# Optimization experiments

Hardware: AMD Instinct MI355X
Metric: run time of the kernel (lower is better)

Reference implementation:

```python
import jax, jax.numpy as jnp
import numpy as np

N = 50000
E_DIR = 200000
KEEP = 320000  # int(0.8 * 2 * E_DIR) after to_undirected + dropout_edge(p=0.2)
IN, OUT, HID = 128, 256, 512
G = 512  # number of graphs
BN_EPS = 1e-5


def setup_inputs() -> dict:
    rng = np.random.default_rng(0)
    x = jnp.asarray(rng.standard_normal((N, IN)).astype(np.float32))
    src = rng.integers(0, N, E_DIR)
    dst = rng.integers(0, N, E_DIR)
    ei = np.stack([src, dst]).astype(np.int64)
    und = np.concatenate([ei, ei[::-1]], axis=1)  # to_undirected -> [2, 2E]
    edge_index1 = jnp.asarray(und[:, rng.permutation(2 * E_DIR)[:KEEP]])
    edge_index2 = jnp.asarray(und[:, rng.permutation(2 * E_DIR)[:KEEP]])
    mask1 = jnp.asarray(rng.permutation(N) < N // 2)
    mask2 = jnp.asarray(rng.permutation(N) < N // 2)
    batch = jnp.asarray(np.sort(rng.integers(0, G, N)).astype(np.int32))

    def w(i, o):
        return jnp.asarray((rng.standard_normal((i, o)) / np.sqrt(i)).astype(np.float32))

    ones = lambda d: jnp.ones((d,), jnp.float32)
    zeros = lambda d: jnp.zeros((d,), jnp.float32)
    return dict(
        x=x, edge_index1=edge_index1, edge_index2=edge_index2,
        mask1=mask1, mask2=mask2, batch=batch,
        e0_w1=w(IN, HID), e0_w2=w(HID, OUT), e0_bg=ones(HID), e0_bb=zeros(HID), e0_ng=ones(OUT), e0_nb=zeros(OUT),
        e1_w1=w(OUT, HID), e1_w2=w(HID, OUT), e1_bg=ones(HID), e1_bb=zeros(HID), e1_ng=ones(OUT), e1_nb=zeros(OUT),
        d_w1=w(OUT, HID), d_w2=w(HID, IN), d_bg=ones(HID), d_bb=zeros(HID), d_ng=ones(IN), d_nb=zeros(IN),
    )


def _bn(h, g, b):  # BatchNorm1d, training mode (batch stats, biased var)
    mu = h.mean(0)
    var = h.var(0)
    return g * (h - mu) * jax.lax.rsqrt(var + BN_EPS) + b


def _gin(xn, ei, w1, w2, bg, bb):
    # GINConv(eps=0): mlp(x + sum_{j in N(i)} x_j); messages flow src->dst
    agg = jax.ops.segment_sum(xn[ei[0]], ei[1], num_segments=xn.shape[0])
    h = xn + agg
    return jax.nn.relu(_bn(h @ w1, bg, bb)) @ w2


def _encoder(xn, ei, batch, layers):
    pooled = []
    for (w1, w2, bg, bb, ng, nb) in layers:
        xn = jax.nn.relu(_bn(_gin(xn, ei, w1, w2, bg, bb), ng, nb))
        pooled.append(jax.ops.segment_sum(xn, batch, num_segments=G))  # global_add_pool
    return xn, jnp.concatenate(pooled, axis=1)


def _cos(a, b):  # F.normalize(p=2) dot product, eps=1e-12
    an = a / jnp.maximum(jnp.linalg.norm(a, axis=-1, keepdims=True), 1e-12)
    bn_ = b / jnp.maximum(jnp.linalg.norm(b, axis=-1, keepdims=True), 1e-12)
    return (an * bn_).sum(-1)


def reference(x, edge_index1, edge_index2, mask1, mask2, batch,
              e0_w1, e0_w2, e0_bg, e0_bb, e0_ng, e0_nb,
              e1_w1, e1_w2, e1_bg, e1_bb, e1_ng, e1_nb,
              d_w1, d_w2, d_bg, d_bb, d_ng, d_nb):
    enc = [(e0_w1, e0_w2, e0_bg, e0_bb, e0_ng, e0_nb),
           (e1_w1, e1_w2, e1_bg, e1_bb, e1_ng, e1_nb)]
    dec = [(d_w1, d_w2, d_bg, d_bb, d_ng, d_nb)]

    def _pass(ei, mb):
        m = mb[:, None]
        x1 = jnp.where(m, 0.0, x)
        h, _gh = _encoder(x1, ei, batch, enc)
        re_h = jnp.where(m, 0.0, h)
        re_x, _ = _encoder(re_h, ei, batch, dec)
        w = mb.astype(x.dtype)
        # sce_loss(alpha=1) restricted to masked rows, target detached
        l = jnp.sum(w * (1.0 - _cos(re_x, jax.lax.stop_gradient(x)))) / jnp.sum(w)
        return re_x, l

    re_x1, loss1 = _pass(edge_index1, mask1)
    re_x2, loss2 = _pass(edge_index2, mask2)
    cl_loss = jnp.mean(1.0 - _cos(re_x2, re_x1))
    return loss1 + loss2 + 0.1 * cl_loss
```

## Files before the change

### kernel.cpp

```cpp
#include <hip/hip_runtime.h>
#include <hip/hip_bf16.h>
#include <cstdint>

#define NN 50000
#define NEDGE 320000

#define K_F32 0
#define K_BF16 1
#define K_IN 2

typedef __attribute__((ext_vector_type(8))) short bf16x8;
typedef __attribute__((ext_vector_type(4))) float f32x4;

__device__ __forceinline__ float bf2f(unsigned short u) {
  return __uint_as_float(((unsigned)u) << 16);
}
__device__ __forceinline__ unsigned short f2bf(float f) {
  unsigned u = __float_as_uint(f);
  unsigned r = ((u >> 16) & 1u) + 0x7FFFu;
  return (unsigned short)((u + r) >> 16);
}
__device__ __forceinline__ float load1f(const void* p, size_t i, int isbf) {
  return isbf ? bf2f(((const unsigned short*)p)[i]) : ((const float*)p)[i];
}
__device__ __forceinline__ int maskAt(const void* m, int i, int u8) {
  return u8 ? (int)((const unsigned char*)m)[i] : ((const int*)m)[i];
}

__global__ void sniff_kernel(const void* bg, const void* mask, const void* ei, int* flags) {
  if (threadIdx.x == 0 && blockIdx.x == 0) {
    unsigned w = *(const unsigned*)bg;
    flags[0] = (w == 0x3F800000u) ? 0 : 1;
    const unsigned char* mb = (const unsigned char*)mask;
    int u8 = 0;
    for (int i = 0; i < 1024; ++i)
      if ((i & 3) && mb[i]) { u8 = 1; break; }
    flags[1] = u8;
    const int* ew = (const int*)ei;
    int i64 = 1;
    for (int i = 0; i < 256; ++i)
      if (ew[2 * i + 1] != 0) { i64 = 0; break; }
    flags[2] = i64;
  }
}

__global__ void diag_kernel(void* out, float v) {
  if (threadIdx.x == 0 && blockIdx.x == 0) ((unsigned short*)out)[0] = f2bf(v);
}

__global__ void transpose_w(const void* __restrict__ W, const int* __restrict__ flags,
                            unsigned short* __restrict__ Wt, int K, int Ko) {
  int idx = blockIdx.x * 256 + threadIdx.x;
  if (idx >= K * Ko) return;
  int n = idx / K, k = idx - n * K;
  Wt[idx] = f2bf(load1f(W, (size_t)k * Ko + n, flags[0]));
}

__global__ void csr_hist(const void* __restrict__ eip, const int* __restrict__ flags,
                         int* __restrict__ deg) {
  int e = blockIdx.x * 256 + threadIdx.x;
  if (e >= NEDGE) return;
  int d = flags[2] ? (int)((const long long*)eip)[NEDGE + e] : ((const int*)eip)[NEDGE + e];
  atomicAdd(deg + d, 1);
}

__global__ void scan1(const int* __restrict__ deg, int* __restrict__ rowptr,
                      int* __restrict__ bsum) {
  __shared__ int sm[256];
  int t = threadIdx.x, i = blockIdx.x * 256 + t;
  int v = (i < NN) ? deg[i] : 0;
  sm[t] = v; __syncthreads();
  for (int o = 1; o < 256; o <<= 1) {
    int y = (t >= o) ? sm[t - o] : 0;
    __syncthreads();
    sm[t] += y;
    __syncthreads();
  }
  if (i < NN) rowptr[i] = sm[t] - v;
  if (t == 255) bsum[blockIdx.x] = sm[255];
}

__global__ void scan2(int* __restrict__ bsum, int nb) {
  __shared__ int sm[256];
  int t = threadIdx.x;
  int v = (t < nb) ? bsum[t] : 0;
  sm[t] = v; __syncthreads();
  for (int o = 1; o < 256; o <<= 1) {
    int y = (t >= o) ? sm[t - o] : 0;
    __syncthreads();
    sm[t] += y;
    __syncthreads();
  }
  bsum[t] = sm[t] - v;
}

__global__ void scan3(int* __restrict__ rowptr, const int* __restrict__ bsum,
                      int* __restrict__ cursor) {
  int i = blockIdx.x * 256 + threadIdx.x;
  if (i < NN) {
    int r = rowptr[i] + bsum[blockIdx.x];
    rowptr[i] = r;
    cursor[i] = r;
  } else if (i == NN) {
    rowptr[NN] = NEDGE;
  }
}

__global__ void csr_fill(const void* __restrict__ eip, const int* __restrict__ flags,
                         int* __restrict__ cursor, int* __restrict__ adj) {
  int e = blockIdx.x * 256 + threadIdx.x;
  if (e >= NEDGE) return;
  int s, d;
  if (flags[2]) {
    s = (int)((const long long*)eip)[e];
    d = (int)((const long long*)eip)[NEDGE + e];
  } else {
    s = ((const int*)eip)[e];
    d = ((const int*)eip)[NEDGE + e];
  }
  int pos = atomicAdd(cursor + d, 1);
  adj[pos] = s;
}

template<int F, bool MASKED, bool BN, bool ISBF>
__device__ __forceinline__ void gf_body(const void* __restrict__ feat,
                                        const void* __restrict__ maskp,
                                        const int* __restrict__ adj,
                                        int s0, int s1, int v, int lane, int mu8,
                                        const float* __restrict__ sc,
                                        const float* __restrict__ sh,
                                        float* __restrict__ a) {
  constexpr int VEC = F / 64;
  auto ld = [&](int r, float* t) {
    size_t gb = (size_t)r * F + lane * VEC;
    if (ISBF) {
      if (VEC == 4) {
        ushort4 h = *(const ushort4*)((const unsigned short*)feat + gb);
        t[0] = bf2f(h.x); t[1] = bf2f(h.y); t[2] = bf2f(h.z); t[3] = bf2f(h.w);
      } else {
        ushort2 h = *(const ushort2*)((const unsigned short*)feat + gb);
        t[0] = bf2f(h.x); t[1] = bf2f(h.y);
      }
    } else {
      if (VEC == 4) {
        float4 h = *(const float4*)((const float*)feat + gb);
        t[0] = h.x; t[1] = h.y; t[2] = h.z; t[3] = h.w;
      } else {
        float2 h = *(const float2*)((const float*)feat + gb);
        t[0] = h.x; t[1] = h.y;
      }
    }
    if (BN) {
#pragma unroll
      for (int i = 0; i < VEC; ++i) t[i] = fmaxf(0.f, t[i] * sc[i] + sh[i]);
    }
  };
  {
    float t[VEC];
    ld(v, t);
    float m = (MASKED && maskAt(maskp, v, mu8)) ? 0.f : 1.f;
#pragma unroll
    for (int i = 0; i < VEC; ++i) a[i] = m * t[i];
  }
  int e = s0;
  for (; e + 4 <= s1; e += 4) {
    int n0 = adj[e], n1 = adj[e + 1], n2 = adj[e + 2], n3 = adj[e + 3];
    float m0 = 1.f, m1 = 1.f, m2 = 1.f, m3 = 1.f;
    if (MASKED) {
      m0 = maskAt(maskp, n0, mu8) ? 0.f : 1.f;
      m1 = maskAt(maskp, n1, mu8) ? 0.f : 1.f;
      m2 = maskAt(maskp, n2, mu8) ? 0.f : 1.f;
      m3 = maskAt(maskp, n3, mu8) ? 0.f : 1.f;
    }
    float t0[VEC], t1[VEC], t2[VEC], t3[VEC];
    ld(n0, t0); ld(n1, t1); ld(n2, t2); ld(n3, t3);
#pragma unroll
    for (int i = 0; i < VEC; ++i)
      a[i] += m0 * t0[i] + m1 * t1[i] + m2 * t2[i] + m3 * t3[i];
  }
  for (; e < s1; ++e) {
    int s = adj[e];
    if (MASKED && maskAt(maskp, s, mu8)) continue;
    float t[VEC];
    ld(s, t);
#pragma unroll
    for (int i = 0; i < VEC; ++i) a[i] += t[i];
  }
}

template<int F, bool MASKED, bool BN>
__launch_bounds__(256)
__global__ void gather_fused(const void* __restrict__ feat, int kind,
                             const void* __restrict__ maskp,
                             const int* __restrict__ rowptr, const int* __restrict__ adj,
                             const float* __restrict__ ss,
                             const int* __restrict__ flags,
                             unsigned short* __restrict__ outH) {
  constexpr int VEC = F / 64;
  int v = (blockIdx.x * 256 + threadIdx.x) >> 6;
  if (v >= NN) return;
  int lane = threadIdx.x & 63;
  int mu8 = flags[1];
  float sc[VEC], sh[VEC];
  if (BN) {
#pragma unroll
    for (int i = 0; i < VEC; ++i) {
      sc[i] = ss[lane * VEC + i];
      sh[i] = ss[F + lane * VEC + i];
    }
  }
  float a[VEC];
  int s0 = rowptr[v], s1 = rowptr[v + 1];
  int fbf = (kind == K_IN) ? flags[0] : kind;
  if (fbf) gf_body<F, MASKED, BN, true>(feat, maskp, adj, s0, s1, v, lane, mu8, sc, sh, a);
  else     gf_body<F, MASKED, BN, false>(feat, maskp, adj, s0, s1, v, lane, mu8, sc, sh, a);
  size_t ob = (size_t)v * F + lane * VEC;
  if (VEC == 4) {
    ushort4 o; o.x = f2bf(a[0]); o.y = f2bf(a[1]); o.z = f2bf(a[2]); o.w = f2bf(a[3]);
    *(ushort4*)(outH + ob) = o;
  } else {
    ushort2 o; o.x = f2bf(a[0]); o.y = f2bf(a[1]);
    *(ushort2*)(outH + ob) = o;
  }
}

template<int K, int KO, int SPLIT, bool BNF>
__launch_bounds__(256)
__global__ void gemm_mfma(const unsigned short* __restrict__ A,
                          const float* __restrict__ ss,
                          const unsigned short* __restrict__ Wt,
                          unsigned short* __restrict__ Cout,
                          float* __restrict__ stats) {
  constexpr int NTW = KO / (SPLIT * 64);
  constexpr int NC = K / 32;
  constexpr int BD = (NTW <= 2) ? 3 : 2;
  __shared__ __align__(16) unsigned short As[2][64 * 40];
  const int tid = threadIdx.x;
  const int row0 = blockIdx.x * 64;
  const int colBase = blockIdx.y * (KO / SPLIT);
  const int srow = tid >> 2;
  const int sk = (tid & 3) * 8;
  const int grow = row0 + srow;
  const bool valid = grow < NN;
  const int wv = tid >> 6, lane = tid & 63;
  const int l15 = lane & 15, quad = lane >> 4;
  const int n0 = colBase + wv * (KO / SPLIT / 4);
  f32x4 zero = {0.f, 0.f, 0.f, 0.f};
  f32x4 acc[4][NTW];
#pragma unroll
  for (int m = 0; m < 4; ++m)
#pragma unroll
    for (int nt = 0; nt < NTW; ++nt) acc[m][nt] = zero;

  ushort4 pbh[2][2];
  bf16x8 breg[BD][NTW];

  auto issue_A = [&](int kt, int set) {
    if (!valid) return;
    const ushort4* P = (const ushort4*)(A + (size_t)grow * K + kt + sk);
    pbh[set][0] = P[0]; pbh[set][1] = P[1];
  };
  auto issue_B = [&](int kt, int buf) {
#pragma unroll
    for (int nt = 0; nt < NTW; ++nt)
      breg[buf][nt] = *(const bf16x8*)(Wt + (size_t)(n0 + nt * 16 + l15) * K + kt + quad * 8);
  };
  auto transform_store = [&](int kt, int set, unsigned short* buf) {
    float v[8];
    if (valid) {
#pragma unroll
      for (int i = 0; i < 2; ++i) {
        v[4 * i] = bf2f(pbh[set][i].x); v[4 * i + 1] = bf2f(pbh[set][i].y);
        v[4 * i + 2] = bf2f(pbh[set][i].z); v[4 * i + 3] = bf2f(pbh[set][i].w);
      }
      if (BNF) {
        int j = kt + sk;
#pragma unroll
        for (int i = 0; i < 8; ++i)
          v[i] = fmaxf(0.f, v[i] * ss[j + i] + ss[K + j + i]);
      }
    } else {
#pragma unroll
      for (int i = 0; i < 8; ++i) v[i] = 0.f;
    }
    unsigned short* dst = buf + srow * 40 + sk;
#pragma unroll
    for (int i = 0; i < 2; ++i) {
      ushort4 o;
      o.x = f2bf(v[4 * i]); o.y = f2bf(v[4 * i + 1]);
      o.z = f2bf(v[4 * i + 2]); o.w = f2bf(v[4 * i + 3]);
      *(ushort4*)(dst + 4 * i) = o;
    }
  };

  issue_A(0, 0);
  transform_store(0, 0, As[0]);
  if (NC > 1) issue_A(32, 1);
  if (NC > 2) issue_A(64, 0);
  issue_B(0, 0);
  if (NC > 1) issue_B(32, 1);
  __syncthreads();

#pragma unroll
  for (int i = 0; i < NC; ++i) {
    const int kt = i << 5;
    if (i + 1 < NC) transform_store(kt + 32, (i + 1) & 1, As[(i + 1) & 1]);
    if (i + 3 < NC) issue_A(kt + 96, (i + 3) & 1);
    if (i + 2 < NC) issue_B(kt + 64, (i + 2) % BD);
    bf16x8 afr[4];
#pragma unroll
    for (int m = 0; m < 4; ++m)
      afr[m] = *(const bf16x8*)(As[i & 1] + (m * 16 + l15) * 40 + quad * 8);
#pragma unroll
    for (int nt = 0; nt < NTW; ++nt)
#pragma unroll
      for (int m = 0; m < 4; ++m)
        acc[m][nt] = __builtin_amdgcn_mfma_f32_16x16x32_bf16(afr[m], breg[i % BD][nt], acc[m][nt], 0, 0, 0);
    __syncthreads();
  }

#pragma unroll
  for (int m = 0; m < 4; ++m)
#pragma unroll
    for (int r = 0; r < 4; ++r) {
      int gr = row0 + m * 16 + quad * 4 + r;
      if (gr < NN) {
        size_t ob = (size_t)gr * KO + n0 + l15;
#pragma unroll
        for (int nt = 0; nt < NTW; ++nt)
          Cout[ob + nt * 16] = f2bf(acc[m][nt][r]);
      }
    }

#pragma unroll
  for (int nt = 0; nt < NTW; ++nt) {
    float s = 0.f, q = 0.f;
#pragma unroll
    for (int m = 0; m < 4; ++m)
#pragma unroll
      for (int r = 0; r < 4; ++r) {
        float vv = acc[m][nt][r];
        s += vv; q += vv * vv;
      }
    s += __shfl_xor(s, 16); s += __shfl_xor(s, 32);
    q += __shfl_xor(q, 16); q += __shfl_xor(q, 32);
    if (quad == 0) {
      int col = n0 + nt * 16 + l15;
      atomicAdd(stats + col, s);
      atomicAdd(stats + KO + col, q);
    }
  }
}

__global__ void bn_finalize(const float* __restrict__ sums, const void* __restrict__ g,
                            const void* __restrict__ b, const int* __restrict__ flags,
                            float* __restrict__ ss, int Ko) {
  int c = blockIdx.x * blockDim.x + threadIdx.x;
  if (c < Ko) {
    const float invN = 1.f / (float)NN;
    float mu = sums[c] * invN;
    float var = sums[Ko + c] * invN - mu * mu;
    float sc = load1f(g, c, flags[0]) * rsqrtf(var + 1e-5f);
    ss[c] = sc;
    ss[Ko + c] = load1f(b, c, flags[0]) - mu * sc;
  }
}

template<bool CL>
__launch_bounds__(256)
__global__ void loss_kernel(const unsigned short* __restrict__ u2, const float* __restrict__ ss,
                            const void* __restrict__ xp, const void* __restrict__ maskp,
                            const unsigned short* __restrict__ r1,
                            const int* __restrict__ flags,
                            unsigned short* __restrict__ rx, float* __restrict__ accb,
                            float* __restrict__ accb_cl) {
  __shared__ float redS[4], redC[4], redL[4];
  const int lane = threadIdx.x & 63;
  const int wv = threadIdx.x >> 6;
  const int g = lane >> 4, li = lane & 15;
  const int r = blockIdx.x * 16 + wv * 4 + g;
  const int fbf = flags[0], mu8 = flags[1];
  const int j0 = li * 8;
  size_t ofs = (size_t)r * 128 + j0;

  float a[8], xv[8], cv[8];
  {
    uint4 h = *(const uint4*)(u2 + ofs);
    unsigned hw[4] = {h.x, h.y, h.z, h.w};
#pragma unroll
    for (int i = 0; i < 4; ++i) {
      a[2 * i]     = bf2f((unsigned short)(hw[i] & 0xFFFF));
      a[2 * i + 1] = bf2f((unsigned short)(hw[i] >> 16));
    }
  }
#pragma unroll
  for (int i = 0; i < 8; ++i)
    a[i] = fmaxf(0.f, a[i] * ss[j0 + i] + ss[128 + j0 + i]);
  {
    uint4 o;
    unsigned ow[4];
#pragma unroll
    for (int i = 0; i < 4; ++i) {
      unsigned short lo = f2bf(a[2 * i]), hi = f2bf(a[2 * i + 1]);
      a[2 * i] = bf2f(lo); a[2 * i + 1] = bf2f(hi);
      ow[i] = (unsigned)lo | ((unsigned)hi << 16);
    }
    o.x = ow[0]; o.y = ow[1]; o.z = ow[2]; o.w = ow[3];
    *(uint4*)(rx + ofs) = o;
  }
  if (fbf) {
    uint4 h = *(const uint4*)((const unsigned short*)xp + ofs);
    unsigned hw[4] = {h.x, h.y, h.z, h.w};
#pragma unroll
    for (int i = 0; i < 4; ++i) {
      xv[2 * i]     = bf2f((unsigned short)(hw[i] & 0xFFFF));
      xv[2 * i + 1] = bf2f((unsigned short)(hw[i] >> 16));
    }
  } else {
    const float* xf = (const float*)xp + ofs;
    float4 h0 = *(const float4*)xf;
    float4 h1 = *(const float4*)(xf + 4);
    xv[0] = h0.x; xv[1] = h0.y; xv[2] = h0.z; xv[3] = h0.w;
    xv[4] = h1.x; xv[5] = h1.y; xv[6] = h1.z; xv[7] = h1.w;
  }
  if (CL) {
    uint4 h = *(const uint4*)(r1 + ofs);
    unsigned hw[4] = {h.x, h.y, h.z, h.w};
#pragma unroll
    for (int i = 0; i < 4; ++i) {
      cv[2 * i]     = bf2f((unsigned short)(hw[i] & 0xFFFF));
      cv[2 * i + 1] = bf2f((unsigned short)(hw[i] >> 16));
    }
  }
  float dot = 0.f, na = 0.f, nx = 0.f, dotc = 0.f, nc = 0.f;
#pragma unroll
  for (int i = 0; i < 8; ++i) {
    dot += a[i] * xv[i];
    na  += a[i] * a[i];
    nx  += xv[i] * xv[i];
    if (CL) { dotc += a[i] * cv[i]; nc += cv[i] * cv[i]; }
  }
#pragma unroll
  for (int off = 1; off < 16; off <<= 1) {
    dot += __shfl_xor(dot, off);
    na  += __shfl_xor(na, off);
    nx  += __shfl_xor(nx, off);
    if (CL) { dotc += __shfl_xor(dotc, off); nc += __shfl_xor(nc, off); }
  }
  float cs = dot / (fmaxf(sqrtf(na), 1e-12f) * fmaxf(sqrtf(nx), 1e-12f));
  float lsum = 0.f, lcnt = 0.f, clsum = 0.f;
  if (maskAt(maskp, r, mu8)) { lsum = 1.f - cs; lcnt = 1.f; }
  if (CL) {
    float csc = dotc / (fmaxf(sqrtf(na), 1e-12f) * fmaxf(sqrtf(nc), 1e-12f));
    clsum = 1.f - csc;
  }
  lsum += __shfl_xor(lsum, 16); lsum += __shfl_xor(lsum, 32);
  lcnt += __shfl_xor(lcnt, 16); lcnt += __shfl_xor(lcnt, 32);
  if (CL) { clsum += __shfl_xor(clsum, 16); clsum += __shfl_xor(clsum, 32); }
  if (lane == 0) { redS[wv] = lsum; redC[wv] = lcnt; if (CL) redL[wv] = clsum; }
  __syncthreads();
  if (threadIdx.x == 0) {
    int bin = (blockIdx.x & 63) * 16;
    atomicAdd(&accb[bin], redS[0] + redS[1] + redS[2] + redS[3]);
    atomicAdd(&accb[1024 + bin], redC[0] + redC[1] + redC[2] + redC[3]);
    if (CL) atomicAdd(&accb_cl[bin], redL[0] + redL[1] + redL[2] + redL[3]);
  }
}

__global__ void final_kernel(const float* __restrict__ acc, void* __restrict__ out,
                             const int* __restrict__ flags) {
  int lane = threadIdx.x & 63;
  float v0 = acc[lane * 16], v1 = acc[1024 + lane * 16], v2 = acc[2048 + lane * 16];
  float v3 = acc[3072 + lane * 16], v4 = acc[4096 + lane * 16];
#pragma unroll
  for (int off = 32; off > 0; off >>= 1) {
    v0 += __shfl_xor(v0, off);
    v1 += __shfl_xor(v1, off);
    v2 += __shfl_xor(v2, off);
    v3 += __shfl_xor(v3, off);
    v4 += __shfl_xor(v4, off);
  }
  if (threadIdx.x == 0 && blockIdx.x == 0) {
    float v = v0 / v1 + v2 / v3 + 0.1f * (v4 / (float)NN);
    if (flags[0]) ((unsigned short*)out)[0] = f2bf(v);
    else          ((float*)out)[0] = v;
  }
}

extern "C" void kernel_launch(void* const* d_in, const int* in_sizes, int n_in,
                              void* d_out, int out_size, void* d_ws, size_t ws_size,
                              hipStream_t stream) {
  const void* x   = d_in[0];
  const void* ei1 = d_in[1];
  const void* ei2 = d_in[2];
  const void* m1  = d_in[3];
  const void* m2  = d_in[4];
  const void* e0_w1 = d_in[6],  *e0_w2 = d_in[7],  *e0_bg = d_in[8],  *e0_bb = d_in[9];
  const void* e0_ng = d_in[10], *e0_nb = d_in[11];
  const void* e1_w1 = d_in[12], *e1_w2 = d_in[13], *e1_bg = d_in[14], *e1_bb = d_in[15];
  const void* e1_ng = d_in[16], *e1_nb = d_in[17];
  const void* dw1 = d_in[18], *dw2 = d_in[19], *dbg = d_in[20], *dbb = d_in[21];
  const void* dng = d_in[22], *dnb = d_in[23];

  char* p = (char*)d_ws;
  const size_t OFS_T      = 0;
  const size_t OFS_H      = OFS_T      + (size_t)NN * 512 * 2;
  const size_t OFS_U      = OFS_H      + (size_t)NN * 256 * 2;
  const size_t OFS_RX1    = OFS_U      + (size_t)NN * 256 * 2;
  const size_t OFS_RX2    = OFS_RX1    + (size_t)NN * 128 * 2;
  const size_t OFS_WT     = OFS_RX2    + (size_t)NN * 128 * 2;
  const size_t OFS_ROWPTR = OFS_WT     + 655360 * 2;
  const size_t OFS_CURSOR = OFS_ROWPTR + 50016 * 4;
  const size_t OFS_ADJ    = OFS_CURSOR + 50016 * 4;
  const size_t OFS_BSUM   = OFS_ADJ    + (size_t)NEDGE * 4;
  const size_t OFS_STATS  = OFS_BSUM   + 256 * 4;
  const size_t OFS_SS     = OFS_STATS  + 6 * 1024 * 4;
  const size_t OFS_ACC    = OFS_SS     + 1024 * 4;
  const size_t OFS_FLAGS  = OFS_ACC    + 5120 * 4;
  const size_t NEED       = OFS_FLAGS + 16;

  if (ws_size < NEED) {
    diag_kernel<<<1, 64, 0, stream>>>(d_out, (float)(ws_size >> 20));
    return;
  }

  unsigned short* T   = (unsigned short*)(p + OFS_T);
  unsigned short* H   = (unsigned short*)(p + OFS_H);
  unsigned short* U   = (unsigned short*)(p + OFS_U);
  unsigned short* RX1 = (unsigned short*)(p + OFS_RX1);
  unsigned short* RX2 = (unsigned short*)(p + OFS_RX2);
  unsigned short* WT  = (unsigned short*)(p + OFS_WT);
  int* rowptr = (int*)(p + OFS_ROWPTR);
  int* cursor = (int*)(p + OFS_CURSOR);
  int* adj    = (int*)(p + OFS_ADJ);
  int* bsum   = (int*)(p + OFS_BSUM);
  float* stats = (float*)(p + OFS_STATS);
  float* ss    = (float*)(p + OFS_SS);
  float* acc   = (float*)(p + OFS_ACC);
  int*   flags = (int*)(p + OFS_FLAGS);

  const int EB = (NEDGE + 255) / 256;
  const int SB = (NN + 255) / 256;
  const int GB = (NN + 63) / 64;
  const int WB = (NN + 3) / 4;
  const int LB = NN / 16;
  const dim3 gS2(GB, 2), gS1(GB, 1);

  hipMemsetAsync(acc, 0, 5120 * sizeof(float) + 4 * sizeof(int), stream);
  sniff_kernel<<<1, 64, 0, stream>>>(e0_bg, m1, ei1, flags);

  transpose_w<<<(128 * 512 + 255) / 256, 256, 0, stream>>>(e0_w1, flags, WT + 0,      128, 512);
  transpose_w<<<(512 * 256 + 255) / 256, 256, 0, stream>>>(e0_w2, flags, WT + 65536,  512, 256);
  transpose_w<<<(256 * 512 + 255) / 256, 256, 0, stream>>>(e1_w1, flags, WT + 196608, 256, 512);
  transpose_w<<<(512 * 256 + 255) / 256, 256, 0, stream>>>(e1_w2, flags, WT + 327680, 512, 256);
  transpose_w<<<(256 * 512 + 255) / 256, 256, 0, stream>>>(dw1,   flags, WT + 458752, 256, 512);
  transpose_w<<<(512 * 128 + 255) / 256, 256, 0, stream>>>(dw2,   flags, WT + 589824, 512, 128);

  for (int pass = 0; pass < 2; ++pass) {
    const void* ei = pass ? ei2 : ei1;
    const void* mk = pass ? m2 : m1;
    unsigned short* rx = pass ? RX2 : RX1;
    float* accp = acc + 2048 * pass;

    hipMemsetAsync(cursor, 0, 50016 * 4, stream);
    csr_hist<<<EB, 256, 0, stream>>>(ei, flags, cursor);
    scan1<<<SB, 256, 0, stream>>>(cursor, rowptr, bsum);
    scan2<<<1, 256, 0, stream>>>(bsum, SB);
    scan3<<<SB, 256, 0, stream>>>(rowptr, bsum, cursor);
    csr_fill<<<EB, 256, 0, stream>>>(ei, flags, cursor, adj);

    hipMemsetAsync(stats, 0, 6 * 1024 * 4, stream);

    gather_fused<128, true, false><<<WB, 256, 0, stream>>>(x, K_IN, mk, rowptr, adj, nullptr, flags, H);
    gemm_mfma<128, 512, 2, false><<<gS2, 256, 0, stream>>>(H, nullptr, WT + 0, T, stats);
    bn_finalize<<<2, 256, 0, stream>>>(stats, e0_bg, e0_bb, flags, ss, 512);
    gemm_mfma<512, 256, 1, true><<<gS1, 256, 0, stream>>>(T, ss, WT + 65536, U, stats + 1024);
    bn_finalize<<<1, 256, 0, stream>>>(stats + 1024, e0_ng, e0_nb, flags, ss, 256);

    gather_fused<256, false, true><<<WB, 256, 0, stream>>>(U, K_BF16, nullptr, rowptr, adj, ss, flags, H);
    gemm_mfma<256, 512, 2, false><<<gS2, 256, 0, stream>>>(H, nullptr, WT + 196608, T, stats + 2048);
    bn_finalize<<<2, 256, 0, stream>>>(stats + 2048, e1_bg, e1_bb, flags, ss, 512);
    gemm_mfma<512, 256, 1, true><<<gS1, 256, 0, stream>>>(T, ss, WT + 327680, U, stats + 3072);
    bn_finalize<<<1, 256, 0, stream>>>(stats + 3072, e1_ng, e1_nb, flags, ss, 256);

    gather_fused<256, true, true><<<WB, 256, 0, stream>>>(U, K_BF16, mk, rowptr, adj, ss, flags, H);
    gemm_mfma<256, 512, 2, false><<<gS2, 256, 0, stream>>>(H, nullptr, WT + 458752, T, stats + 4096);
    bn_finalize<<<2, 256, 0, stream>>>(stats + 4096, dbg, dbb, flags, ss, 512);
    gemm_mfma<512, 128, 1, true><<<gS1, 256, 0, stream>>>(T, ss, WT + 589824, U, stats + 5120);
    bn_finalize<<<1, 256, 0, stream>>>(stats + 5120, dng, dnb, flags, ss, 128);

    if (pass == 0)
      loss_kernel<false><<<LB, 256, 0, stream>>>(U, ss, x, mk, nullptr, flags, rx, accp, nullptr);
    else
      loss_kernel<true><<<LB, 256, 0, stream>>>(U, ss, x, mk, RX1, flags, rx, accp, acc + 4096);
  }

  final_kernel<<<1, 64, 0, stream>>>(acc, d_out, flags);
}
```

Measured before the change: 1.171 ms.

## Batch both augmentation passes into single kernel launches over stacked rows

Runs the two independent encoder/decoder passes together. Each CSR build, gather, GEMM and BN-finalize launch now covers both passes, with per-pass offsets into doubled row buffers padded to a multiple of 64 rows. The two separate loss kernels become one that computes both reconstruction losses and the contrastive term in a single read, so the re-x buffers are no longer written and read back. This halves the number of launches and doubles grid sizes for better GPU fill, at the cost of twice the workspace memory.

```diff
diff --git a/kernel.cpp b/kernel.cpp
--- a/kernel.cpp
+++ b/kernel.cpp
@@ -3,7 +3,11 @@
 #include <cstdint>
 
 #define NN 50000
+#define NNP 50048
 #define NEDGE 320000
+#define PB (NNP / 64)
+#define EBV 1250
+#define SBV 196
 
 #define K_F32 0
 #define K_BF16 1
@@ -25,6 +29,14 @@
 }
 __device__ __forceinline__ int maskAt(const void* m, int i, int u8) {
   return u8 ? (int)((const unsigned char*)m)[i] : ((const int*)m)[i];
+}
+__device__ __forceinline__ void unpack8(uint4 h, float* t) {
+  unsigned hw[4] = {h.x, h.y, h.z, h.w};
+#pragma unroll
+  for (int i = 0; i < 4; ++i) {
+    t[2 * i]     = bf2f((unsigned short)(hw[i] & 0xFFFF));
+    t[2 * i + 1] = bf2f((unsigned short)(hw[i] >> 16));
+  }
 }
 
 __global__ void sniff_kernel(const void* bg, const void* mask, const void* ei, int* flags) {
@@ -56,19 +68,24 @@
   Wt[idx] = f2bf(load1f(W, (size_t)k * Ko + n, flags[0]));
 }
 
-__global__ void csr_hist(const void* __restrict__ eip, const int* __restrict__ flags,
-                         int* __restrict__ deg) {
-  int e = blockIdx.x * 256 + threadIdx.x;
-  if (e >= NEDGE) return;
+__global__ void csr_hist(const void* __restrict__ e1, const void* __restrict__ e2,
+                         const int* __restrict__ flags, int* __restrict__ deg2) {
+  int eg = blockIdx.x * 256 + threadIdx.x;
+  int p = eg >= NEDGE ? 1 : 0;
+  int e = eg - p * NEDGE;
+  const void* eip = p ? e2 : e1;
   int d = flags[2] ? (int)((const long long*)eip)[NEDGE + e] : ((const int*)eip)[NEDGE + e];
-  atomicAdd(deg + d, 1);
-}
-
-__global__ void scan1(const int* __restrict__ deg, int* __restrict__ rowptr,
-                      int* __restrict__ bsum) {
+  atomicAdd(deg2 + p * 50016 + d, 1);
+}
+
+__global__ void scan1(const int* __restrict__ deg2, int* __restrict__ rowptr2,
+                      int* __restrict__ bsum2) {
   __shared__ int sm[256];
-  int t = threadIdx.x, i = blockIdx.x * 256 + t;
-  int v = (i < NN) ? deg[i] : 0;
+  int t = threadIdx.x;
+  int p = blockIdx.x >= SBV ? 1 : 0;
+  int b = blockIdx.x - p * SBV;
+  int i = b * 256 + t;
+  int v = (i < NN) ? deg2[p * 50016 + i] : 0;
   sm[t] = v; __syncthreads();
   for (int o = 1; o < 256; o <<= 1) {
     int y = (t >= o) ? sm[t - o] : 0;
@@ -76,14 +93,15 @@
     sm[t] += y;
     __syncthreads();
   }
-  if (i < NN) rowptr[i] = sm[t] - v;
-  if (t == 255) bsum[blockIdx.x] = sm[255];
-}
-
-__global__ void scan2(int* __restrict__ bsum, int nb) {
+  if (i < NN) rowptr2[p * 50016 + i] = sm[t] - v;
+  if (t == 255) bsum2[p * 256 + b] = sm[255];
+}
+
+__global__ void scan2(int* __restrict__ bsum2) {
   __shared__ int sm[256];
   int t = threadIdx.x;
-  int v = (t < nb) ? bsum[t] : 0;
+  int* arr = bsum2 + blockIdx.x * 256;
+  int v = (t < SBV) ? arr[t] : 0;
   sm[t] = v; __syncthreads();
   for (int o = 1; o < 256; o <<= 1) {
     int y = (t >= o) ? sm[t - o] : 0;
@@ -91,25 +109,30 @@
     sm[t] += y;
     __syncthreads();
   }
-  bsum[t] = sm[t] - v;
-}
-
-__global__ void scan3(int* __restrict__ rowptr, const int* __restrict__ bsum,
-                      int* __restrict__ cursor) {
-  int i = blockIdx.x * 256 + threadIdx.x;
+  arr[t] = sm[t] - v;
+}
+
+__global__ void scan3(int* __restrict__ rowptr2, const int* __restrict__ bsum2,
+                      int* __restrict__ cursor2) {
+  int p = blockIdx.x >= SBV ? 1 : 0;
+  int b = blockIdx.x - p * SBV;
+  int i = b * 256 + threadIdx.x;
   if (i < NN) {
-    int r = rowptr[i] + bsum[blockIdx.x];
-    rowptr[i] = r;
-    cursor[i] = r;
+    int r = rowptr2[p * 50016 + i] + bsum2[p * 256 + b];
+    rowptr2[p * 50016 + i] = r;
+    cursor2[p * 50016 + i] = r;
   } else if (i == NN) {
-    rowptr[NN] = NEDGE;
-  }
-}
-
-__global__ void csr_fill(const void* __restrict__ eip, const int* __restrict__ flags,
-                         int* __restrict__ cursor, int* __restrict__ adj) {
-  int e = blockIdx.x * 256 + threadIdx.x;
-  if (e >= NEDGE) return;
+    rowptr2[p * 50016 + NN] = NEDGE;
+  }
+}
+
+__global__ void csr_fill(const void* __restrict__ e1, const void* __restrict__ e2,
+                         const int* __restrict__ flags,
+                         int* __restrict__ cursor2, int* __restrict__ adj2) {
+  int eg = blockIdx.x * 256 + threadIdx.x;
+  int p = eg >= NEDGE ? 1 : 0;
+  int e = eg - p * NEDGE;
+  const void* eip = p ? e2 : e1;
   int s, d;
   if (flags[2]) {
     s = (int)((const long long*)eip)[e];
@@ -118,21 +141,23 @@
     s = ((const int*)eip)[e];
     d = ((const int*)eip)[NEDGE + e];
   }
-  int pos = atomicAdd(cursor + d, 1);
-  adj[pos] = s;
-}
-
-template<int F, bool MASKED, bool BN, bool ISBF>
+  int pos = atomicAdd(cursor2 + p * 50016 + d, 1);
+  adj2[p * NEDGE + pos] = s;
+}
+
+template<int F, bool MASKED, bool BN, bool ISBF, bool SHARED>
 __device__ __forceinline__ void gf_body(const void* __restrict__ feat,
                                         const void* __restrict__ maskp,
                                         const int* __restrict__ adj,
-                                        int s0, int s1, int v, int lane, int mu8,
+                                        int s0, int s1, int v, size_t pbase,
+                                        int lane, int mu8,
                                         const float* __restrict__ sc,
                                         const float* __restrict__ sh,
                                         float* __restrict__ a) {
   constexpr int VEC = F / 64;
   auto ld = [&](int r, float* t) {
-    size_t gb = (size_t)r * F + lane * VEC;
+    size_t frow = SHARED ? (size_t)r : (pbase + r);
+    size_t gb = frow * F + lane * VEC;
     if (ISBF) {
       if (VEC == 4) {
         ushort4 h = *(const ushort4*)((const unsigned short*)feat + gb);
@@ -188,33 +213,39 @@
   }
 }
 
-template<int F, bool MASKED, bool BN>
+template<int F, bool MASKED, bool BN, bool SHARED>
 __launch_bounds__(256)
 __global__ void gather_fused(const void* __restrict__ feat, int kind,
-                             const void* __restrict__ maskp,
-                             const int* __restrict__ rowptr, const int* __restrict__ adj,
+                             const void* __restrict__ mk1, const void* __restrict__ mk2,
+                             const int* __restrict__ rowptr2, const int* __restrict__ adj2,
                              const float* __restrict__ ss,
                              const int* __restrict__ flags,
                              unsigned short* __restrict__ outH) {
   constexpr int VEC = F / 64;
-  int v = (blockIdx.x * 256 + threadIdx.x) >> 6;
-  if (v >= NN) return;
+  int w = (blockIdx.x * 256 + threadIdx.x) >> 6;
+  int p = w >= NN ? 1 : 0;
+  int v = w - p * NN;
   int lane = threadIdx.x & 63;
   int mu8 = flags[1];
+  const void* mk = p ? mk2 : mk1;
+  const int* rp_ = rowptr2 + p * 50016;
+  const int* aj = adj2 + p * NEDGE;
+  const float* ssp = ss + p * 2 * F;
+  size_t pbase = (size_t)p * NNP;
   float sc[VEC], sh[VEC];
   if (BN) {
 #pragma unroll
     for (int i = 0; i < VEC; ++i) {
-      sc[i] = ss[lane * VEC + i];
-      sh[i] = ss[F + lane * VEC + i];
+      sc[i] = ssp[lane * VEC + i];
+      sh[i] = ssp[F + lane * VEC + i];
     }
   }
   float a[VEC];
-  int s0 = rowptr[v], s1 = rowptr[v + 1];
+  int s0 = rp_[v], s1 = rp_[v + 1];
   int fbf = (kind == K_IN) ? flags[0] : kind;
-  if (fbf) gf_body<F, MASKED, BN, true>(feat, maskp, adj, s0, s1, v, lane, mu8, sc, sh, a);
-  else     gf_body<F, MASKED, BN, false>(feat, maskp, adj, s0, s1, v, lane, mu8, sc, sh, a);
-  size_t ob = (size_t)v * F + lane * VEC;
+  if (fbf) gf_body<F, MASKED, BN, true, SHARED>(feat, mk, aj, s0, s1, v, pbase, lane, mu8, sc, sh, a);
+  else     gf_body<F, MASKED, BN, false, SHARED>(feat, mk, aj, s0, s1, v, pbase, lane, mu8, sc, sh, a);
+  size_t ob = (pbase + v) * F + lane * VEC;
   if (VEC == 4) {
     ushort4 o; o.x = f2bf(a[0]); o.y = f2bf(a[1]); o.z = f2bf(a[2]); o.w = f2bf(a[3]);
     *(ushort4*)(outH + ob) = o;
@@ -236,15 +267,18 @@
   constexpr int BD = (NTW <= 2) ? 3 : 2;
   __shared__ __align__(16) unsigned short As[2][64 * 40];
   const int tid = threadIdx.x;
+  const int pass = (blockIdx.x >= PB) ? 1 : 0;
   const int row0 = blockIdx.x * 64;
   const int colBase = blockIdx.y * (KO / SPLIT);
   const int srow = tid >> 2;
   const int sk = (tid & 3) * 8;
   const int grow = row0 + srow;
-  const bool valid = grow < NN;
+  const bool valid = (grow - pass * NNP) < NN;
   const int wv = tid >> 6, lane = tid & 63;
   const int l15 = lane & 15, quad = lane >> 4;
   const int n0 = colBase + wv * (KO / SPLIT / 4);
+  const float* ssp = BNF ? (ss + pass * 2 * K) : ss;
+  float* statsp = stats + pass * 1024;
   f32x4 zero = {0.f, 0.f, 0.f, 0.f};
   f32x4 acc[4][NTW];
 #pragma unroll
@@ -277,7 +311,7 @@
         int j = kt + sk;
 #pragma unroll
         for (int i = 0; i < 8; ++i)
-          v[i] = fmaxf(0.f, v[i] * ss[j + i] + ss[K + j + i]);
+          v[i] = fmaxf(0.f, v[i] * ssp[j + i] + ssp[K + j + i]);
       }
     } else {
 #pragma unroll
@@ -324,7 +358,7 @@
 #pragma unroll
     for (int r = 0; r < 4; ++r) {
       int gr = row0 + m * 16 + quad * 4 + r;
-      if (gr < NN) {
+      if (gr - pass * NNP < NN) {
         size_t ob = (size_t)gr * KO + n0 + l15;
 #pragma unroll
         for (int nt = 0; nt < NTW; ++nt)
@@ -346,8 +380,8 @@
     q += __shfl_xor(q, 16); q += __shfl_xor(q, 32);
     if (quad == 0) {
       int col = n0 + nt * 16 + l15;
-      atomicAdd(stats + col, s);
-      atomicAdd(stats + KO + col, q);
+      atomicAdd(statsp + col, s);
+      atomicAdd(statsp + KO + col, q);
     }
   }
 }
@@ -356,114 +390,91 @@
                             const void* __restrict__ b, const int* __restrict__ flags,
                             float* __restrict__ ss, int Ko) {
   int c = blockIdx.x * blockDim.x + threadIdx.x;
+  int p = blockIdx.y;
   if (c < Ko) {
     const float invN = 1.f / (float)NN;
-    float mu = sums[c] * invN;
-    float var = sums[Ko + c] * invN - mu * mu;
+    float mu = sums[p * 1024 + c] * invN;
+    float var = sums[p * 1024 + Ko + c] * invN - mu * mu;
     float sc = load1f(g, c, flags[0]) * rsqrtf(var + 1e-5f);
-    ss[c] = sc;
-    ss[Ko + c] = load1f(b, c, flags[0]) - mu * sc;
-  }
-}
-
-template<bool CL>
+    ss[p * 2 * Ko + c] = sc;
+    ss[p * 2 * Ko + Ko + c] = load1f(b, c, flags[0]) - mu * sc;
+  }
+}
+
 __launch_bounds__(256)
-__global__ void loss_kernel(const unsigned short* __restrict__ u2, const float* __restrict__ ss,
-                            const void* __restrict__ xp, const void* __restrict__ maskp,
-                            const unsigned short* __restrict__ r1,
-                            const int* __restrict__ flags,
-                            unsigned short* __restrict__ rx, float* __restrict__ accb,
-                            float* __restrict__ accb_cl) {
-  __shared__ float redS[4], redC[4], redL[4];
+__global__ void loss_all(const unsigned short* __restrict__ U2, const float* __restrict__ ss,
+                         const void* __restrict__ xp,
+                         const void* __restrict__ mk1, const void* __restrict__ mk2,
+                         const int* __restrict__ flags, float* __restrict__ accb) {
+  __shared__ float r1S[4], r1C[4], r2S[4], r2C[4], rL[4];
   const int lane = threadIdx.x & 63;
   const int wv = threadIdx.x >> 6;
   const int g = lane >> 4, li = lane & 15;
-  const int r = blockIdx.x * 16 + wv * 4 + g;
+  const int v = blockIdx.x * 16 + wv * 4 + g;
   const int fbf = flags[0], mu8 = flags[1];
   const int j0 = li * 8;
-  size_t ofs = (size_t)r * 128 + j0;
-
-  float a[8], xv[8], cv[8];
-  {
-    uint4 h = *(const uint4*)(u2 + ofs);
-    unsigned hw[4] = {h.x, h.y, h.z, h.w};
-#pragma unroll
-    for (int i = 0; i < 4; ++i) {
-      a[2 * i]     = bf2f((unsigned short)(hw[i] & 0xFFFF));
-      a[2 * i + 1] = bf2f((unsigned short)(hw[i] >> 16));
-    }
-  }
-#pragma unroll
-  for (int i = 0; i < 8; ++i)
-    a[i] = fmaxf(0.f, a[i] * ss[j0 + i] + ss[128 + j0 + i]);
-  {
-    uint4 o;
-    unsigned ow[4];
-#pragma unroll
-    for (int i = 0; i < 4; ++i) {
-      unsigned short lo = f2bf(a[2 * i]), hi = f2bf(a[2 * i + 1]);
-      a[2 * i] = bf2f(lo); a[2 * i + 1] = bf2f(hi);
-      ow[i] = (unsigned)lo | ((unsigned)hi << 16);
-    }
-    o.x = ow[0]; o.y = ow[1]; o.z = ow[2]; o.w = ow[3];
-    *(uint4*)(rx + ofs) = o;
+  size_t o1 = (size_t)v * 128 + j0;
+  size_t o2 = ((size_t)NNP + v) * 128 + j0;
+
+  float a1[8], a2[8], xv[8];
+  unpack8(*(const uint4*)(U2 + o1), a1);
+  unpack8(*(const uint4*)(U2 + o2), a2);
+#pragma unroll
+  for (int i = 0; i < 8; ++i) {
+    a1[i] = fmaxf(0.f, a1[i] * ss[j0 + i]       + ss[128 + j0 + i]);
+    a2[i] = fmaxf(0.f, a2[i] * ss[256 + j0 + i] + ss[384 + j0 + i]);
+    a1[i] = bf2f(f2bf(a1[i]));
+    a2[i] = bf2f(f2bf(a2[i]));
   }
   if (fbf) {
-    uint4 h = *(const uint4*)((const unsigned short*)xp + ofs);
-    unsigned hw[4] = {h.x, h.y, h.z, h.w};
-#pragma unroll
-    for (int i = 0; i < 4; ++i) {
-      xv[2 * i]     = bf2f((unsigned short)(hw[i] & 0xFFFF));
-      xv[2 * i + 1] = bf2f((unsigned short)(hw[i] >> 16));
-    }
+    unpack8(*(const uint4*)((const unsigned short*)xp + o1), xv);
   } else {
-    const float* xf = (const float*)xp + ofs;
+    const float* xf = (const float*)xp + o1;
     float4 h0 = *(const float4*)xf;
     float4 h1 = *(const float4*)(xf + 4);
     xv[0] = h0.x; xv[1] = h0.y; xv[2] = h0.z; xv[3] = h0.w;
     xv[4] = h1.x; xv[5] = h1.y; xv[6] = h1.z; xv[7] = h1.w;
   }
-  if (CL) {
-    uint4 h = *(const uint4*)(r1 + ofs);
-    unsigned hw[4] = {h.x, h.y, h.z, h.w};
-#pragma unroll
-    for (int i = 0; i < 4; ++i) {
-      cv[2 * i]     = bf2f((unsigned short)(hw[i] & 0xFFFF));
-      cv[2 * i + 1] = bf2f((unsigned short)(hw[i] >> 16));
-    }
-  }
-  float dot = 0.f, na = 0.f, nx = 0.f, dotc = 0.f, nc = 0.f;
+  float d1 = 0.f, d2 = 0.f, dc = 0.f, n1 = 0.f, n2 = 0.f, nx = 0.f;
 #pragma unroll
   for (int i = 0; i < 8; ++i) {
-    dot += a[i] * xv[i];
-    na  += a[i] * a[i];
-    nx  += xv[i] * xv[i];
-    if (CL) { dotc += a[i] * cv[i]; nc += cv[i] * cv[i]; }
+    d1 += a1[i] * xv[i];
+    d2 += a2[i] * xv[i];
+    dc += a2[i] * a1[i];
+    n1 += a1[i] * a1[i];
+    n2 += a2[i] * a2[i];
+    nx += xv[i] * xv[i];
   }
 #pragma unroll
   for (int off = 1; off < 16; off <<= 1) {
-    dot += __shfl_xor(dot, off);
-    na  += __shfl_xor(na, off);
-    nx  += __shfl_xor(nx, off);
-    if (CL) { dotc += __shfl_xor(dotc, off); nc += __shfl_xor(nc, off); }
-  }
-  float cs = dot / (fmaxf(sqrtf(na), 1e-12f) * fmaxf(sqrtf(nx), 1e-12f));
-  float lsum = 0.f, lcnt = 0.f, clsum = 0.f;
-  if (maskAt(maskp, r, mu8)) { lsum = 1.f - cs; lcnt = 1.f; }
-  if (CL) {
-    float csc = dotc / (fmaxf(sqrtf(na), 1e-12f) * fmaxf(sqrtf(nc), 1e-12f));
-    clsum = 1.f - csc;
-  }
-  lsum += __shfl_xor(lsum, 16); lsum += __shfl_xor(lsum, 32);
-  lcnt += __shfl_xor(lcnt, 16); lcnt += __shfl_xor(lcnt, 32);
-  if (CL) { clsum += __shfl_xor(clsum, 16); clsum += __shfl_xor(clsum, 32); }
-  if (lane == 0) { redS[wv] = lsum; redC[wv] = lcnt; if (CL) redL[wv] = clsum; }
+    d1 += __shfl_xor(d1, off);
+    d2 += __shfl_xor(d2, off);
+    dc += __shfl_xor(dc, off);
+    n1 += __shfl_xor(n1, off);
+    n2 += __shfl_xor(n2, off);
+    nx += __shfl_xor(nx, off);
+  }
+  float s1 = fmaxf(sqrtf(n1), 1e-12f), s2 = fmaxf(sqrtf(n2), 1e-12f);
+  float sx = fmaxf(sqrtf(nx), 1e-12f);
+  float cs1 = d1 / (s1 * sx), cs2 = d2 / (s2 * sx), csc = dc / (s2 * s1);
+  float l1 = 0.f, c1 = 0.f, l2 = 0.f, c2 = 0.f;
+  if (maskAt(mk1, v, mu8)) { l1 = 1.f - cs1; c1 = 1.f; }
+  if (maskAt(mk2, v, mu8)) { l2 = 1.f - cs2; c2 = 1.f; }
+  float cl = 1.f - csc;
+  l1 += __shfl_xor(l1, 16); l1 += __shfl_xor(l1, 32);
+  c1 += __shfl_xor(c1, 16); c1 += __shfl_xor(c1, 32);
+  l2 += __shfl_xor(l2, 16); l2 += __shfl_xor(l2, 32);
+  c2 += __shfl_xor(c2, 16); c2 += __shfl_xor(c2, 32);
+  cl += __shfl_xor(cl, 16); cl += __shfl_xor(cl, 32);
+  if (lane == 0) { r1S[wv] = l1; r1C[wv] = c1; r2S[wv] = l2; r2C[wv] = c2; rL[wv] = cl; }
   __syncthreads();
   if (threadIdx.x == 0) {
     int bin = (blockIdx.x & 63) * 16;
-    atomicAdd(&accb[bin], redS[0] + redS[1] + redS[2] + redS[3]);
-    atomicAdd(&accb[1024 + bin], redC[0] + redC[1] + redC[2] + redC[3]);
-    if (CL) atomicAdd(&accb_cl[bin], redL[0] + redL[1] + redL[2] + redL[3]);
+    atomicAdd(&accb[bin],        r1S[0] + r1S[1] + r1S[2] + r1S[3]);
+    atomicAdd(&accb[1024 + bin], r1C[0] + r1C[1] + r1C[2] + r1C[3]);
+    atomicAdd(&accb[2048 + bin], r2S[0] + r2S[1] + r2S[2] + r2S[3]);
+    atomicAdd(&accb[3072 + bin], r2C[0] + r2C[1] + r2C[2] + r2C[3]);
+    atomicAdd(&accb[4096 + bin], rL[0] + rL[1] + rL[2] + rL[3]);
   }
 }
 
@@ -503,19 +514,18 @@
   const void* dng = d_in[22], *dnb = d_in[23];
 
   char* p = (char*)d_ws;
+  const size_t NR = 2 * (size_t)NNP;
   const size_t OFS_T      = 0;
-  const size_t OFS_H      = OFS_T      + (size_t)NN * 512 * 2;
-  const size_t OFS_U      = OFS_H      + (size_t)NN * 256 * 2;
-  const size_t OFS_RX1    = OFS_U      + (size_t)NN * 256 * 2;
-  const size_t OFS_RX2    = OFS_RX1    + (size_t)NN * 128 * 2;
-  const size_t OFS_WT     = OFS_RX2    + (size_t)NN * 128 * 2;
+  const size_t OFS_H      = OFS_T      + NR * 512 * 2;
+  const size_t OFS_U      = OFS_H      + NR * 256 * 2;
+  const size_t OFS_WT     = OFS_U      + NR * 256 * 2;
   const size_t OFS_ROWPTR = OFS_WT     + 655360 * 2;
-  const size_t OFS_CURSOR = OFS_ROWPTR + 50016 * 4;
-  const size_t OFS_ADJ    = OFS_CURSOR + 50016 * 4;
-  const size_t OFS_BSUM   = OFS_ADJ    + (size_t)NEDGE * 4;
-  const size_t OFS_STATS  = OFS_BSUM   + 256 * 4;
-  const size_t OFS_SS     = OFS_STATS  + 6 * 1024 * 4;
-  const size_t OFS_ACC    = OFS_SS     + 1024 * 4;
+  const size_t OFS_CURSOR = OFS_ROWPTR + 2 * 50016 * 4;
+  const size_t OFS_ADJ    = OFS_CURSOR + 2 * 50016 * 4;
+  const size_t OFS_BSUM   = OFS_ADJ    + 2 * (size_t)NEDGE * 4;
+  const size_t OFS_STATS  = OFS_BSUM   + 512 * 4;
+  const size_t OFS_SS     = OFS_STATS  + 12 * 1024 * 4;
+  const size_t OFS_ACC    = OFS_SS     + 2048 * 4;
   const size_t OFS_FLAGS  = OFS_ACC    + 5120 * 4;
   const size_t NEED       = OFS_FLAGS + 16;
 
@@ -527,26 +537,24 @@
   unsigned short* T   = (unsigned short*)(p + OFS_T);
   unsigned short* H   = (unsigned short*)(p + OFS_H);
   unsigned short* U   = (unsigned short*)(p + OFS_U);
-  unsigned short* RX1 = (unsigned short*)(p + OFS_RX1);
-  unsigned short* RX2 = (unsigned short*)(p + OFS_RX2);
   unsigned short* WT  = (unsigned short*)(p + OFS_WT);
-  int* rowptr = (int*)(p + OFS_ROWPTR);
-  int* cursor = (int*)(p + OFS_CURSOR);
-  int* adj    = (int*)(p + OFS_ADJ);
-  int* bsum   = (int*)(p + OFS_BSUM);
+  int* rowptr2 = (int*)(p + OFS_ROWPTR);
+  int* cursor2 = (int*)(p + OFS_CURSOR);
+  int* adj2    = (int*)(p + OFS_ADJ);
+  int* bsum2   = (int*)(p + OFS_BSUM);
   float* stats = (float*)(p + OFS_STATS);
   float* ss    = (float*)(p + OFS_SS);
   float* acc   = (float*)(p + OFS_ACC);
   int*   flags = (int*)(p + OFS_FLAGS);
 
-  const int EB = (NEDGE + 255) / 256;
-  const int SB = (NN + 255) / 256;
-  const int GB = (NN + 63) / 64;
-  const int WB = (NN + 3) / 4;
-  const int LB = NN / 16;
-  const dim3 gS2(GB, 2), gS1(GB, 1);
-
-  hipMemsetAsync(acc, 0, 5120 * sizeof(float) + 4 * sizeof(int), stream);
+  const int GB2 = 2 * PB;
+  const int WB2 = 2 * NN / 4;
+  const int LB  = NN / 16;
+  const dim3 gS2(GB2, 2), gS1(GB2, 1);
+  const dim3 bn512((512 + 255) / 256, 2), bn256(1, 2), bn128(1, 2);
+
+  hipMemsetAsync(stats, 0, (12 * 1024 + 2048 + 5120) * 4 + 16, stream);
+  hipMemsetAsync(cursor2, 0, 2 * 50016 * 4, stream);
   sniff_kernel<<<1, 64, 0, stream>>>(e0_bg, m1, ei1, flags);
 
   transpose_w<<<(128 * 512 + 255) / 256, 256, 0, stream>>>(e0_w1, flags, WT + 0,      128, 512);
@@ -556,44 +564,33 @@
   transpose_w<<<(256 * 512 + 255) / 256, 256, 0, stream>>>(dw1,   flags, WT + 458752, 256, 512);
   transpose_w<<<(512 * 128 + 255) / 256, 256, 0, stream>>>(dw2,   flags, WT + 589824, 512, 128);
 
-  for (int pass = 0; pass < 2; ++pass) {
-    const void* ei = pass ? ei2 : ei1;
-    const void* mk = pass ? m2 : m1;
-    unsigned short* rx = pass ? RX2 : RX1;
-    float* accp = acc + 2048 * pass;
-
-    hipMemsetAsync(cursor, 0, 50016 * 4, stream);
-    csr_hist<<<EB, 256, 0, stream>>>(ei, flags, cursor);
-    scan1<<<SB, 256, 0, stream>>>(cursor, rowptr, bsum);
-    scan2<<<1, 256, 0, stream>>>(bsum, SB);
-    scan3<<<SB, 256, 0, stream>>>(rowptr, bsum, cursor);
-    csr_fill<<<EB, 256, 0, stream>>>(ei, flags, cursor, adj);
-
-    hipMemsetAsync(stats, 0, 6 * 1024 * 4, stream);
-
-    gather_fused<128, true, false><<<WB, 256, 0, stream>>>(x, K_IN, mk, rowptr, adj, nullptr, flags, H);
-    gemm_mfma<128, 512, 2, false><<<gS2, 256, 0, stream>>>(H, nullptr, WT + 0, T, stats);
-    bn_finalize<<<2, 256, 0, stream>>>(stats, e0_bg, e0_bb, flags, ss, 512);
-    gemm_mfma<512, 256, 1, true><<<gS1, 256, 0, stream>>>(T, ss, WT + 65536, U, stats + 1024);
-    bn_finalize<<<1, 256, 0, stream>>>(stats + 1024, e0_ng, e0_nb, flags, ss, 256);
-
-    gather_fused<256, false, true><<<WB, 256, 0, stream>>>(U, K_BF16, nullptr, rowptr, adj, ss, flags, H);
-    gemm_mfma<256, 512, 2, false><<<gS2, 256, 0, stream>>>(H, nullptr, WT + 196608, T, stats + 2048);
-    bn_finalize<<<2, 256, 0, stream>>>(stats + 2048, e1_bg, e1_bb, flags, ss, 512);
-    gemm_mfma<512, 256, 1, true><<<gS1, 256, 0, stream>>>(T, ss, WT + 327680, U, stats + 3072);
-    bn_finalize<<<1, 256, 0, stream>>>(stats + 3072, e1_ng, e1_nb, flags, ss, 256);
-
-    gather_fused<256, true, true><<<WB, 256, 0, stream>>>(U, K_BF16, mk, rowptr, adj, ss, flags, H);
-    gemm_mfma<256, 512, 2, false><<<gS2, 256, 0, stream>>>(H, nullptr, WT + 458752, T, stats + 4096);
-    bn_finalize<<<2, 256, 0, stream>>>(stats + 4096, dbg, dbb, flags, ss, 512);
-    gemm_mfma<512, 128, 1, true><<<gS1, 256, 0, stream>>>(T, ss, WT + 589824, U, stats + 5120);
-    bn_finalize<<<1, 256, 0, stream>>>(stats + 5120, dng, dnb, flags, ss, 128);
-
-    if (pass == 0)
-      loss_kernel<false><<<LB, 256, 0, stream>>>(U, ss, x, mk, nullptr, flags, rx, accp, nullptr);
-    else
-      loss_kernel<true><<<LB, 256, 0, stream>>>(U, ss, x, mk, RX1, flags, rx, accp, acc + 4096);
-  }
-
+  csr_hist<<<2 * EBV, 256, 0, stream>>>(ei1, ei2, flags, cursor2);
+  scan1<<<2 * SBV, 256, 0, stream>>>(cursor2, rowptr2, bsum2);
+  scan2<<<2, 256, 0, stream>>>(bsum2);
+  scan3<<<2 * SBV, 256, 0, stream>>>(rowptr2, bsum2, cursor2);
+  csr_fill<<<2 * EBV, 256, 0, stream>>>(ei1, ei2, flags, cursor2, adj2);
+
+  gather_fused<128, true, false, true><<<WB2, 256, 0, stream>>>(
+      x, K_IN, m1, m2, rowptr2, adj2, nullptr, flags, H);
+  gemm_mfma<128, 512, 2, false><<<gS2, 256, 0, stream>>>(H, nullptr, WT + 0, T, stats);
+  bn_finalize<<<bn512, 256, 0, stream>>>(stats, e0_bg, e0_bb, flags, ss, 512);
+  gemm_mfma<512, 256, 1, true><<<gS1, 256, 0, stream>>>(T, ss, WT + 65536, U, stats + 2048);
+  bn_finalize<<<bn256, 256, 0, stream>>>(stats + 2048, e0_ng, e0_nb, flags, ss, 256);
+
+  gather_fused<256, false, true, false><<<WB2, 256, 0, stream>>>(
+      U, K_BF16, nullptr, nullptr, rowptr2, adj2, ss, flags, H);
+  gemm_mfma<256, 512, 2, false><<<gS2, 256, 0, stream>>>(H, nullptr, WT + 196608, T, stats + 4096);
+  bn_finalize<<<bn512, 256, 0, stream>>>(stats + 4096, e1_bg, e1_bb, flags, ss, 512);
+  gemm_mfma<512, 256, 1, true><<<gS1, 256, 0, stream>>>(T, ss, WT + 327680, U, stats + 6144);
+  bn_finalize<<<bn256, 256, 0, stream>>>(stats + 6144, e1_ng, e1_nb, flags, ss, 256);
+
+  gather_fused<256, true, true, false><<<WB2, 256, 0, stream>>>(
+      U, K_BF16, m1, m2, rowptr2, adj2, ss, flags, H);
+  gemm_mfma<256, 512, 2, false><<<gS2, 256, 0, stream>>>(H, nullptr, WT + 458752, T, stats + 8192);
+  bn_finalize<<<bn512, 256, 0, stream>>>(stats + 8192, dbg, dbb, flags, ss, 512);
+  gemm_mfma<512, 128, 1, true><<<gS1, 256, 0, stream>>>(T, ss, WT + 589824, U, stats + 10240);
+  bn_finalize<<<bn128, 256, 0, stream>>>(stats + 10240, dng, dnb, flags, ss, 128);
+
+  loss_all<<<LB, 256, 0, stream>>>(U, ss, x, m1, m2, flags, acc);
   final_kernel<<<1, 64, 0, stream>>>(acc, d_out, flags);
 }
```

Result: faster. 1.000 ms (-14.6%).
